# Kernel tuning notes

Hardware: AMD Instinct MI355X
Metric: run time of the kernel (lower is better)

Reference implementation:

```python
import jax, jax.numpy as jnp
import numpy as np

SLOPE = 25.0   # surrogate.fast_sigmoid(slope=25)
THRESH = 1.0   # snntorch default threshold
BN_EPS = 1e-5
LN_EPS = 1e-5

@jax.custom_vjp
def spike(x):
    return (x > 0).astype(x.dtype)

def _spike_fwd(x):
    return (x > 0).astype(x.dtype), x

def _spike_bwd(x, g):
    # fast_sigmoid surrogate gradient: 1 / (slope*|x| + 1)^2
    return (g / (SLOPE * jnp.abs(x) + 1.0) ** 2,)

spike.defvjp(_spike_fwd, _spike_bwd)

def lif(inp, mem, beta):
    # snntorch Leaky (reset_mechanism='subtract'):
    # reset from previous mem, then integrate, then fire
    reset = spike(mem - THRESH)
    mem = beta * mem + inp - reset * THRESH
    spk = spike(mem - THRESH)
    return spk, mem

def _forward(L_norm, X_seq, conv_w, conv_b, bn_gamma, bn_beta, bn_mean, bn_var,
             gcn1_w, gcn1_b, mask1, gcn2_w, gcn2_b, mask2, beta2,
             attn_w1, attn_b1, attn_w2, attn_b2,
             cls_w1, cls_b1, ln_gamma, ln_beta, cls_w2, cls_b2):
    B = X_seq.shape[0]
    N = L_norm.shape[1]            # 64 nodes
    # [B,T,N,1] -> [B,N,T]
    x = jnp.squeeze(X_seq, -1).transpose(0, 2, 1)
    # causal conv1d (pad left k-1=2) + inference BatchNorm1d
    y = jax.lax.conv_general_dilated(x, conv_w, (1,), [(2, 0)],
                                     dimension_numbers=('NCH', 'OIH', 'NCH'))
    y = y + conv_b[None, :, None]
    y = (y - bn_mean[None, :, None]) * (bn_gamma[None, :, None]
        * jax.lax.rsqrt(bn_var[None, :, None] + BN_EPS)) + bn_beta[None, :, None]
    # dynamic Laplacian masks (constant across steps -> hoisted out of scan)
    m1 = jax.nn.sigmoid(mask1 + mask1.T) * 0.5
    m2 = jax.nn.sigmoid(mask2 + mask2.T) * 0.5
    L1 = L_norm * m1[None]         # [B,N,N]
    L2 = L_norm * m2[None]
    xs = y.transpose(2, 0, 1)[..., None]   # [T,B,N,1]

    def step(carry, xt):
        mem_t, mem_g1, mem_g2 = carry
        spk_t, mem_t = lif(xt, mem_t, 0.9)
        cur1 = jnp.einsum('bij,bjf->bif', L1, spk_t @ gcn1_w) + gcn1_b
        spk1, mem_g1 = lif(cur1, mem_g1, 0.85)
        cur2 = jnp.einsum('bij,bjf->bif', L2, spk1 @ gcn2_w) + gcn2_b
        spk2, mem_g2 = lif(cur2, mem_g2, beta2)
        return (mem_t, mem_g1, mem_g2), mem_g2.reshape(B, -1)

    init = (jnp.zeros((B, N, 1), x.dtype),
            jnp.zeros((B, N, 16), x.dtype),
            jnp.zeros((B, N, 32), x.dtype))
    _, pots = jax.lax.scan(step, init, xs)       # [T,B,N*32]
    pots = pots.transpose(1, 0, 2)               # [B,T,2048]
    # temporal attention decoder
    scores = jnp.tanh(pots @ attn_w1 + attn_b1) @ attn_w2 + attn_b2  # [B,T,1]
    w = jax.nn.softmax(scores, axis=1)
    ctx = jnp.sum(pots * w, axis=1)              # [B,2048]
    h = ctx @ cls_w1 + cls_b1                    # [B,128]
    mu = jnp.mean(h, axis=-1, keepdims=True)
    var = jnp.var(h, axis=-1, keepdims=True)
    h = (h - mu) * jax.lax.rsqrt(var + LN_EPS) * ln_gamma + ln_beta
    h = jax.nn.gelu(h, approximate=False)        # dropout is identity at eval
    return h @ cls_w2 + cls_b2                   # [B,4]

def setup_inputs() -> dict:
    key = jax.random.key(0)
    ks = jax.random.split(key, 16)
    B, T, N = 4096, 15, 64
    f32 = jnp.float32
    def xavier(k, shape):
        lim = float(np.sqrt(6.0 / (shape[0] + shape[1])))
        return jax.random.uniform(k, shape, f32, -lim, lim)
    return {
        'L_norm': jax.random.normal(ks[0], (B, N, N), f32),
        'X_seq': jax.random.normal(ks[1], (B, T, N, 1), f32),
        'conv_w': jax.random.normal(ks[2], (64, 64, 3), f32) / np.sqrt(64 * 3),
        'conv_b': jnp.zeros((64,), f32),
        'bn_gamma': jnp.ones((64,), f32),
        'bn_beta': jnp.zeros((64,), f32),
        'bn_mean': jnp.zeros((64,), f32),
        'bn_var': jnp.ones((64,), f32),
        'gcn1_w': xavier(ks[3], (1, 16)),
        'gcn1_b': jnp.zeros((16,), f32),
        'mask1': jnp.ones((N, N), f32),
        'gcn2_w': xavier(ks[4], (16, 32)),
        'gcn2_b': jnp.zeros((32,), f32),
        'mask2': jnp.ones((N, N), f32),
        'beta2': jnp.asarray(0.9, f32),
        'attn_w1': xavier(ks[5], (2048, 32)),
        'attn_b1': jnp.zeros((32,), f32),
        'attn_w2': xavier(ks[6], (32, 1)),
        'attn_b2': jnp.zeros((1,), f32),
        'cls_w1': xavier(ks[7], (2048, 128)),
        'cls_b1': jnp.zeros((128,), f32),
        'ln_gamma': jnp.ones((128,), f32),
        'ln_beta': jnp.zeros((128,), f32),
        'cls_w2': xavier(ks[8], (128, 4)),
        'cls_b2': jnp.zeros((4,), f32),
    }

def reference(L_norm, X_seq, conv_w, conv_b, bn_gamma, bn_beta, bn_mean, bn_var,
              gcn1_w, gcn1_b, mask1, gcn2_w, gcn2_b, mask2, beta2,
              attn_w1, attn_b1, attn_w2, attn_b2,
              cls_w1, cls_b1, ln_gamma, ln_beta, cls_w2, cls_b2):
    return _forward(L_norm, X_seq, conv_w, conv_b, bn_gamma, bn_beta, bn_mean, bn_var,
                    gcn1_w, gcn1_b, mask1, gcn2_w, gcn2_b, mask2, beta2,
                    attn_w1, attn_b1, attn_w2, attn_b2,
                    cls_w1, cls_b1, ln_gamma, ln_beta, cls_w2, cls_b2)
```

## Files before the change

### kernel.cpp

```cpp
#include <hip/hip_runtime.h>
#include <math.h>

#define WS_M1_F    0
#define WS_M2_F    4096
#define WS_BNSC_F  8192
#define WS_BNSH_F  8256
#define WS_WT_F    8448
#define OFF_W1T    83968
#define OFF_CW1H   215040
#define OFF_CW1L   739328
#define OFF_CTX    1263616

typedef _Float16 v8h __attribute__((ext_vector_type(8)));
typedef short v8s __attribute__((ext_vector_type(8)));
typedef float v4f __attribute__((ext_vector_type(4)));
typedef float v16f __attribute__((ext_vector_type(16)));

__device__ __forceinline__ unsigned short f2h_u(float x) {
  _Float16 h = (_Float16)x;
  union { _Float16 h; unsigned short u; } v; v.h = h; return v.u;
}
__device__ __forceinline__ unsigned short bf16t(float x) {
  union { float f; unsigned int u; } v; v.f = x; return (unsigned short)(v.u >> 16);
}
__device__ __forceinline__ float bf16tof(unsigned short s) {
  union { unsigned int u; float f; } v; v.u = ((unsigned int)s) << 16; return v.f;
}

__global__ __launch_bounds__(256) void k_prep(
    const float* __restrict__ mask1, const float* __restrict__ mask2,
    const float* __restrict__ conv_w, const float* __restrict__ conv_b,
    const float* __restrict__ bn_gamma, const float* __restrict__ bn_beta,
    const float* __restrict__ bn_mean, const float* __restrict__ bn_var,
    const float* __restrict__ attn_w1, const float* __restrict__ cls_w1,
    float* __restrict__ wsf, unsigned short* __restrict__ w1t,
    unsigned short* __restrict__ cw1h, unsigned short* __restrict__ cw1l)
{
  const int gid = blockIdx.x * 256 + threadIdx.x;
  const int gsz = gridDim.x * 256;
  float* m1 = wsf + WS_M1_F;
  float* m2 = wsf + WS_M2_F;
  float* bnsc = wsf + WS_BNSC_F;
  float* bnsh = wsf + WS_BNSH_F;
  float* wT = wsf + WS_WT_F;
  for (int e = gid; e < 4096; e += gsz) {
    int i = e >> 6, j = e & 63;
    float s1 = mask1[e] + mask1[j * 64 + i];
    float s2 = mask2[e] + mask2[j * 64 + i];
    m1[e] = 0.5f / (1.f + expf(-s1));
    m2[e] = 0.5f / (1.f + expf(-s2));
  }
  for (int e = gid; e < 64; e += gsz) {
    float sc = bn_gamma[e] * rsqrtf(bn_var[e] + 1e-5f);
    bnsc[e] = sc;
    bnsh[e] = (conv_b[e] - bn_mean[e]) * sc + bn_beta[e];
  }
  for (int e = gid; e < 12288; e += gsz) {
    int o = e / 192, ik = e % 192;
    wT[ik * 64 + o] = conv_w[e];
  }
  for (int e = gid; e < 65536; e += gsz) {
    int n = e >> 11, i = e & 2047;
    w1t[e] = f2h_u(attn_w1[i * 32 + n]);
  }
  for (int e = gid; e < 262144; e += gsz) {
    int n = e >> 11, k = e & 2047;
    float x = cls_w1[k * 128 + n];
    unsigned short h = bf16t(x);
    cw1h[e] = h;
    cw1l[e] = bf16t(x - bf16tof(h));
  }
}

__global__ __launch_bounds__(256) void k_fused(
    const float* __restrict__ L_norm, const float* __restrict__ X_seq,
    const float* __restrict__ gcn1_w, const float* __restrict__ gcn1_b,
    const float* __restrict__ gcn2_w, const float* __restrict__ gcn2_b,
    const float* __restrict__ beta2p, const float* __restrict__ wsf,
    const unsigned short* __restrict__ w1t,
    const float* __restrict__ attn_b1, const float* __restrict__ attn_w2,
    const float* __restrict__ attn_b2,
    unsigned short* __restrict__ ctxh, unsigned short* __restrict__ ctxl,
    int b0)
{
  __shared__ __align__(16) unsigned short pots_s[16 * 2048];
  __shared__ __align__(16) char smR[11776];
  float* xcur = (float*)smR;
  float* zp = (float*)(smR + 3840);
  unsigned short* spk1T = (unsigned short*)(smR + 4352);
  float* Z2f = (float*)(smR + 6656);

  const int tid = threadIdx.x;
  const int lane = tid & 63;
  const int wv = tid >> 6;
  const int b = b0 + blockIdx.x;

  const float* m1 = wsf + WS_M1_F;
  const float* m2 = wsf + WS_M2_F;

  {
    float* xraw = (float*)pots_s;
    for (int e = tid; e < 960; e += 256) xraw[e] = X_seq[(size_t)b * 960 + e];
    *(uint4*)&pots_s[15 * 2048 + tid * 8] = make_uint4(0u, 0u, 0u, 0u);
    __syncthreads();
    const float* bnsc = wsf + WS_BNSC_F;
    const float* bnsh = wsf + WS_BNSH_F;
    const float* wT = wsf + WS_WT_F;
    const int o = lane;
    const int t0 = wv, t1 = wv + 4, t2 = wv + 8, t3 = wv + 12;
    float a0 = 0.f, a1 = 0.f, a2 = 0.f, a3 = 0.f;
    for (int i = 0; i < 64; ++i) {
      const float w0 = wT[(3 * i + 0) * 64 + o];
      const float w1 = wT[(3 * i + 1) * 64 + o];
      const float w2 = wT[(3 * i + 2) * 64 + o];
      float xa = (t0 >= 2) ? xraw[(t0 - 2) * 64 + i] : 0.f;
      float xb = (t0 >= 1) ? xraw[(t0 - 1) * 64 + i] : 0.f;
      a0 += w0 * xa + w1 * xb + w2 * xraw[t0 * 64 + i];
      a1 += w0 * xraw[(t1 - 2) * 64 + i] + w1 * xraw[(t1 - 1) * 64 + i] + w2 * xraw[t1 * 64 + i];
      a2 += w0 * xraw[(t2 - 2) * 64 + i] + w1 * xraw[(t2 - 1) * 64 + i] + w2 * xraw[t2 * 64 + i];
      if (t3 < 15)
        a3 += w0 * xraw[(t3 - 2) * 64 + i] + w1 * xraw[(t3 - 1) * 64 + i] + w2 * xraw[t3 * 64 + i];
    }
    const float sc = bnsc[o], sh = bnsh[o];
    xcur[t0 * 64 + o] = a0 * sc + sh;
    xcur[t1 * 64 + o] = a1 * sc + sh;
    xcur[t2 * 64 + o] = a2 * sc + sh;
    if (t3 < 15) xcur[t3 * 64 + o] = a3 * sc + sh;
    __syncthreads();
  }

  float L1h[32];
  const int kb1 = (wv & 1) * 32;
  if (wv >= 2) {
    const float* Lb = L_norm + (size_t)b * 4096 + lane * 64 + kb1;
    const float* mr = m1 + lane * 64 + kb1;
#pragma unroll
    for (int q4 = 0; q4 < 8; ++q4) {
      float4 lv = *(const float4*)(Lb + 4 * q4);
      float4 mv = *(const float4*)(mr + 4 * q4);
      L1h[4 * q4 + 0] = lv.x * mv.x;
      L1h[4 * q4 + 1] = lv.y * mv.y;
      L1h[4 * q4 + 2] = lv.z * mv.z;
      L1h[4 * q4 + 3] = lv.w * mv.w;
    }
  }

  v8s A_hi[2], A_lo[2];
  {
    const int irow = wv * 16 + (lane & 15);
    const int quad = (lane >> 4) & 3;
#pragma unroll
    for (int kb = 0; kb < 2; ++kb) {
      const float* Lb = L_norm + (size_t)b * 4096 + irow * 64 + kb * 32 + quad * 8;
      const float* mr = m2 + irow * 64 + kb * 32 + quad * 8;
      float4 la = *(const float4*)Lb, lb2 = *(const float4*)(Lb + 4);
      float4 ma = *(const float4*)mr, mb = *(const float4*)(mr + 4);
      float v[8] = { la.x * ma.x, la.y * ma.y, la.z * ma.z, la.w * ma.w,
                     lb2.x * mb.x, lb2.y * mb.y, lb2.z * mb.z, lb2.w * mb.w };
#pragma unroll
      for (int e = 0; e < 8; ++e) {
        unsigned short h = bf16t(v[e]);
        unsigned short l = bf16t(v[e] - bf16tof(h));
        A_hi[kb][e] = (short)h;
        A_lo[kb][e] = (short)l;
      }
    }
  }

  v8s W_hi, W_lo;
  {
    const int n = lane & 31;
    const int kh = (lane >> 5) & 1;
#pragma unroll
    for (int e = 0; e < 8; ++e) {
      float x = gcn2_w[(kh * 8 + e) * 32 + n];
      unsigned short h = bf16t(x);
      unsigned short l = bf16t(x - bf16tof(h));
      W_hi[e] = (short)h;
      W_lo[e] = (short)l;
    }
  }

  const float b2h = gcn2_b[lane & 31];
  const int np = tid >> 3;
  const int cp = tid & 7;
  float w1c[2], b1c[2];
#pragma unroll
  for (int d = 0; d < 2; ++d) { w1c[d] = gcn1_w[2 * cp + d]; b1c[d] = gcn1_b[2 * cp + d]; }
  const float beta2 = beta2p[0];

  float mem_t = 0.f;
  float mg1[4] = {0.f, 0.f, 0.f, 0.f};
  v16f mg2;
#pragma unroll
  for (int r = 0; r < 16; ++r) mg2[r] = 0.f;

  auto stage_b = [&](int tm1) {
    const int m = lane & 31;
    const int half = lane >> 5;
    const float* zr = Z2f + (wv * 32 + m) * 20 + half * 8;
    float4 za = *(const float4*)zr;
    float4 zb = *(const float4*)(zr + 4);
    float vv[8] = {za.x, za.y, za.z, za.w, zb.x, zb.y, zb.z, zb.w};
    v8s Ah, Al;
#pragma unroll
    for (int e = 0; e < 8; ++e) {
      unsigned short h = bf16t(vv[e]);
      unsigned short l = bf16t(vv[e] - bf16tof(h));
      Ah[e] = (short)h;
      Al[e] = (short)l;
    }
    v16f acc;
#pragma unroll
    for (int r = 0; r < 16; ++r) {
      float rs = (mg2[r] > 1.f) ? 1.f : 0.f;
      acc[r] = fmaf(beta2, mg2[r], b2h - rs);
    }
    acc = __builtin_amdgcn_mfma_f32_32x32x16_bf16(Ah, W_hi, acc, 0, 0, 0);
    acc = __builtin_amdgcn_mfma_f32_32x32x16_bf16(Al, W_hi, acc, 0, 0, 0);
    acc = __builtin_amdgcn_mfma_f32_32x32x16_bf16(Ah, W_lo, acc, 0, 0, 0);
    mg2 = acc;
    const int xorv = (tm1 & 7) << 3;
    const int base = tm1 * 2048 + m;
#pragma unroll
    for (int r = 0; r < 16; ++r) {
      int i = wv * 32 + (r & 3) + 8 * (r >> 2) + 4 * half;
      pots_s[(base + i * 32) ^ xorv] = f2h_u(acc[r]);
    }
  };

  for (int t = 0; t < 15; ++t) {
    if (wv >= 2) {
      float xc = xcur[t * 64 + lane];
      float rs = (mem_t > 1.f) ? 1.f : 0.f;
      mem_t = 0.9f * mem_t + xc - rs;
      float sp = (mem_t > 1.f) ? 1.f : 0.f;
      int spi = __float_as_int(sp);
      float zh = 0.f;
#pragma unroll
      for (int k = 0; k < 32; ++k) {
        float s = __int_as_float(__builtin_amdgcn_readlane(spi, kb1 + k));
        zh = fmaf(s, L1h[k], zh);
      }
      zp[(wv & 1) * 64 + lane] = zh;
    } else if (t > 0) {
      stage_b(t - 1);
    }
    __syncthreads();
    {
      float2 q0 = *(const float2*)&zp[2 * np];
      float2 q1 = *(const float2*)&zp[64 + 2 * np];
      float z0 = q0.x + q1.x;
      float z1v = q0.y + q1.y;
#pragma unroll
      for (int d = 0; d < 2; ++d) {
        float cur0 = fmaf(z0, w1c[d], b1c[d]);
        float rs0 = (mg1[d * 2 + 0] > 1.f) ? 1.f : 0.f;
        mg1[d * 2 + 0] = 0.85f * mg1[d * 2 + 0] + cur0 - rs0;
        unsigned int bits0 = (mg1[d * 2 + 0] > 1.f) ? 0x3F80u : 0u;
        float cur1 = fmaf(z1v, w1c[d], b1c[d]);
        float rs1 = (mg1[d * 2 + 1] > 1.f) ? 1.f : 0.f;
        mg1[d * 2 + 1] = 0.85f * mg1[d * 2 + 1] + cur1 - rs1;
        unsigned int bits1 = (mg1[d * 2 + 1] > 1.f) ? 0x3F80u : 0u;
        *(unsigned int*)&spk1T[(2 * cp + d) * 72 + 2 * np] = bits0 | (bits1 << 16);
      }
    }
    __syncthreads();
    {
      const int c = lane & 15;
      const int quad = (lane >> 4) & 3;
      const unsigned short* bp = spk1T + c * 72 + quad * 8;
      v8s B0 = *(const v8s*)(bp);
      v8s B1 = *(const v8s*)(bp + 32);
      v4f acc = {0.f, 0.f, 0.f, 0.f};
      acc = __builtin_amdgcn_mfma_f32_16x16x32_bf16(A_hi[0], B0, acc, 0, 0, 0);
      acc = __builtin_amdgcn_mfma_f32_16x16x32_bf16(A_lo[0], B0, acc, 0, 0, 0);
      acc = __builtin_amdgcn_mfma_f32_16x16x32_bf16(A_hi[1], B1, acc, 0, 0, 0);
      acc = __builtin_amdgcn_mfma_f32_16x16x32_bf16(A_lo[1], B1, acc, 0, 0, 0);
      const int r0 = wv * 16 + quad * 4;
#pragma unroll
      for (int r = 0; r < 4; ++r) Z2f[(r0 + r) * 20 + c] = acc[r];
    }
    __syncthreads();
  }
  if (wv < 2) stage_b(14);
  __syncthreads();

  float* sred = (float*)smR;
  float* wbuf = (float*)(smR + 8192);
  const int m = lane & 15;
  const int quad = lane >> 4;
  const int koff = quad * 8;

  v4f a0 = {0.f, 0.f, 0.f, 0.f}, a1 = {0.f, 0.f, 0.f, 0.f};
  {
    const int axor = (m & 7) << 3;
    const int abase = m * 2048 + koff;
    const unsigned short* B0p = w1t + (size_t)m * 2048 + koff;
    const unsigned short* B1p = w1t + (size_t)(m + 16) * 2048 + koff;
#pragma unroll 4
    for (int c = wv * 16; c < wv * 16 + 16; ++c) {
      v8h A = *(const v8h*)(pots_s + ((abase + c * 32) ^ axor));
      v8h B0 = *(const v8h*)(B0p + c * 32);
      v8h B1 = *(const v8h*)(B1p + c * 32);
      a0 = __builtin_amdgcn_mfma_f32_16x16x32_f16(A, B0, a0, 0, 0, 0);
      a1 = __builtin_amdgcn_mfma_f32_16x16x32_f16(A, B1, a1, 0, 0, 0);
    }
  }
#pragma unroll
  for (int j = 0; j < 4; ++j) {
    sred[j * 256 + tid] = a0[j];
    sred[(j + 4) * 256 + tid] = a1[j];
  }
  __syncthreads();
  float s0[4], s1[4];
#pragma unroll
  for (int j = 0; j < 4; ++j) {
    s0[j] = sred[j * 256 + 0 * 64 + lane] + sred[j * 256 + 1 * 64 + lane]
          + sred[j * 256 + 2 * 64 + lane] + sred[j * 256 + 3 * 64 + lane];
    s1[j] = sred[(j + 4) * 256 + 0 * 64 + lane] + sred[(j + 4) * 256 + 1 * 64 + lane]
          + sred[(j + 4) * 256 + 2 * 64 + lane] + sred[(j + 4) * 256 + 3 * 64 + lane];
  }
  float wlar[16];
  {
    const int n = m;
    const float b1a = attn_b1[n], b1b = attn_b1[n + 16];
    const float w2a = attn_w2[n], w2b = attn_w2[n + 16];
    const float b2 = attn_b2[0];
    float sc[4];
#pragma unroll
    for (int r = 0; r < 4; ++r) {
      float v = tanhf(s0[r] + b1a) * w2a + tanhf(s1[r] + b1b) * w2b;
      v += __shfl_xor(v, 1, 64);
      v += __shfl_xor(v, 2, 64);
      v += __shfl_xor(v, 4, 64);
      v += __shfl_xor(v, 8, 64);
      sc[r] = v + b2;
    }
    float mx = -1e30f;
#pragma unroll
    for (int r = 0; r < 4; ++r) if (quad * 4 + r < 15) mx = fmaxf(mx, sc[r]);
    mx = fmaxf(mx, __shfl_xor(mx, 16, 64));
    mx = fmaxf(mx, __shfl_xor(mx, 32, 64));
    float e[4], den = 0.f;
#pragma unroll
    for (int r = 0; r < 4; ++r) {
      e[r] = (quad * 4 + r < 15) ? expf(sc[r] - mx) : 0.f;
      den += e[r];
    }
    den += __shfl_xor(den, 16, 64);
    den += __shfl_xor(den, 32, 64);
    const float inv = 1.f / den;
    if ((lane & 15) == 0) {
      v4f wq = {e[0] * inv, e[1] * inv, e[2] * inv, e[3] * inv};
      *(v4f*)&wbuf[wv * 16 + quad * 4] = wq;
    }
#pragma unroll
    for (int q4 = 0; q4 < 4; ++q4) {
      float4 v = *(const float4*)&wbuf[wv * 16 + q4 * 4];
      wlar[q4 * 4 + 0] = v.x; wlar[q4 * 4 + 1] = v.y;
      wlar[q4 * 4 + 2] = v.z; wlar[q4 * 4 + 3] = v.w;
    }
  }
  float cv[8] = {0.f, 0.f, 0.f, 0.f, 0.f, 0.f, 0.f, 0.f};
#pragma unroll
  for (int t = 0; t < 15; ++t) {
    const int idx = (t * 2048 + tid * 8) ^ ((t & 7) << 3);
    v8h pv = *(const v8h*)(pots_s + idx);
    const float w = wlar[t];
#pragma unroll
    for (int j = 0; j < 8; ++j) cv[j] = fmaf(w, (float)pv[j], cv[j]);
  }
  unsigned short hv[8], lv[8];
#pragma unroll
  for (int j = 0; j < 8; ++j) {
    unsigned short h = bf16t(cv[j]);
    hv[j] = h;
    lv[j] = bf16t(cv[j] - bf16tof(h));
  }
  *(uint4*)(ctxh + (size_t)blockIdx.x * 2048 + tid * 8) = *(const uint4*)hv;
  *(uint4*)(ctxl + (size_t)blockIdx.x * 2048 + tid * 8) = *(const uint4*)lv;
}

__global__ __launch_bounds__(256) void k_cls(
    const unsigned short* __restrict__ ctxh, const unsigned short* __restrict__ ctxl,
    const unsigned short* __restrict__ cw1h, const unsigned short* __restrict__ cw1l,
    const float* __restrict__ cls_b1,
    const float* __restrict__ ln_g, const float* __restrict__ ln_b,
    const float* __restrict__ cls_w2, const float* __restrict__ cls_b2,
    float* __restrict__ out, int b0)
{
  __shared__ float hbuf[16 * 132];
  const int tid = threadIdx.x;
  const int lane = tid & 63;
  const int wv = tid >> 6;
  const int m = lane & 15;
  const int quad = lane >> 4;
  const int koff = quad * 8;
  const int r0l = blockIdx.x * 16;

  v4f a0 = {0.f, 0.f, 0.f, 0.f}, a1 = {0.f, 0.f, 0.f, 0.f};
  {
    const unsigned short* Ah = ctxh + (size_t)(r0l + m) * 2048;
    const unsigned short* Al = ctxl + (size_t)(r0l + m) * 2048;
    const int n0 = wv * 32 + m;
    const unsigned short* B0h = cw1h + (size_t)n0 * 2048;
    const unsigned short* B0l = cw1l + (size_t)n0 * 2048;
    const unsigned short* B1h = cw1h + (size_t)(n0 + 16) * 2048;
    const unsigned short* B1l = cw1l + (size_t)(n0 + 16) * 2048;
#pragma unroll 4
    for (int kc = 0; kc < 64; ++kc) {
      const int kb = kc * 32 + koff;
      v8s vAh = *(const v8s*)(Ah + kb);
      v8s vAl = *(const v8s*)(Al + kb);
      v8s vB0h = *(const v8s*)(B0h + kb);
      v8s vB0l = *(const v8s*)(B0l + kb);
      v8s vB1h = *(const v8s*)(B1h + kb);
      v8s vB1l = *(const v8s*)(B1l + kb);
      a0 = __builtin_amdgcn_mfma_f32_16x16x32_bf16(vAh, vB0h, a0, 0, 0, 0);
      a0 = __builtin_amdgcn_mfma_f32_16x16x32_bf16(vAl, vB0h, a0, 0, 0, 0);
      a0 = __builtin_amdgcn_mfma_f32_16x16x32_bf16(vAh, vB0l, a0, 0, 0, 0);
      a1 = __builtin_amdgcn_mfma_f32_16x16x32_bf16(vAh, vB1h, a1, 0, 0, 0);
      a1 = __builtin_amdgcn_mfma_f32_16x16x32_bf16(vAl, vB1h, a1, 0, 0, 0);
      a1 = __builtin_amdgcn_mfma_f32_16x16x32_bf16(vAh, vB1l, a1, 0, 0, 0);
    }
  }
  {
    const int n0 = wv * 32 + m;
    const float bb0 = cls_b1[n0], bb1 = cls_b1[n0 + 16];
#pragma unroll
    for (int r = 0; r < 4; ++r) {
      const int row = quad * 4 + r;
      hbuf[row * 132 + n0] = a0[r] + bb0;
      hbuf[row * 132 + n0 + 16] = a1[r] + bb1;
    }
  }
  __syncthreads();
  const float g0c = ln_g[lane], g1c = ln_g[lane + 64];
  const float b0c = ln_b[lane], b1c = ln_b[lane + 64];
  const float4 w2a = *(const float4*)(cls_w2 + lane * 4);
  const float4 w2b = *(const float4*)(cls_w2 + (lane + 64) * 4);
#pragma unroll
  for (int rr = 0; rr < 4; ++rr) {
    const int r = wv * 4 + rr;
    const float x0 = hbuf[r * 132 + lane];
    const float x1 = hbuf[r * 132 + 64 + lane];
    float s = x0 + x1, sq = x0 * x0 + x1 * x1;
#pragma unroll
    for (int mm = 32; mm >= 1; mm >>= 1) {
      s += __shfl_xor(s, mm, 64);
      sq += __shfl_xor(sq, mm, 64);
    }
    const float mu = s * (1.f / 128.f);
    const float var = sq * (1.f / 128.f) - mu * mu;
    const float rstd = rsqrtf(var + 1e-5f);
    float h0 = (x0 - mu) * rstd * g0c + b0c;
    float h1 = (x1 - mu) * rstd * g1c + b1c;
    h0 = 0.5f * h0 * (1.f + erff(h0 * 0.7071067811865475f));
    h1 = 0.5f * h1 * (1.f + erff(h1 * 0.7071067811865475f));
    float o0 = h0 * w2a.x + h1 * w2b.x;
    float o1 = h0 * w2a.y + h1 * w2b.y;
    float o2 = h0 * w2a.z + h1 * w2b.z;
    float o3 = h0 * w2a.w + h1 * w2b.w;
#pragma unroll
    for (int mm = 32; mm >= 1; mm >>= 1) {
      o0 += __shfl_xor(o0, mm, 64);
      o1 += __shfl_xor(o1, mm, 64);
      o2 += __shfl_xor(o2, mm, 64);
      o3 += __shfl_xor(o3, mm, 64);
    }
    if (lane == 0) {
      *(float4*)(out + (size_t)(b0 + r0l + r) * 4) =
          make_float4(o0 + cls_b2[0], o1 + cls_b2[1], o2 + cls_b2[2], o3 + cls_b2[3]);
    }
  }
}

extern "C" void kernel_launch(void* const* d_in, const int* in_sizes, int n_in,
                              void* d_out, int out_size, void* d_ws, size_t ws_size,
                              hipStream_t stream) {
  const float* L_norm   = (const float*)d_in[0];
  const float* X_seq    = (const float*)d_in[1];
  const float* conv_w   = (const float*)d_in[2];
  const float* conv_b   = (const float*)d_in[3];
  const float* bn_gamma = (const float*)d_in[4];
  const float* bn_beta  = (const float*)d_in[5];
  const float* bn_mean  = (const float*)d_in[6];
  const float* bn_var   = (const float*)d_in[7];
  const float* gcn1_w   = (const float*)d_in[8];
  const float* gcn1_b   = (const float*)d_in[9];
  const float* mask1    = (const float*)d_in[10];
  const float* gcn2_w   = (const float*)d_in[11];
  const float* gcn2_b   = (const float*)d_in[12];
  const float* mask2    = (const float*)d_in[13];
  const float* beta2    = (const float*)d_in[14];
  const float* attn_w1  = (const float*)d_in[15];
  const float* attn_b1  = (const float*)d_in[16];
  const float* attn_w2  = (const float*)d_in[17];
  const float* attn_b2  = (const float*)d_in[18];
  const float* cls_w1   = (const float*)d_in[19];
  const float* cls_b1   = (const float*)d_in[20];
  const float* ln_gamma = (const float*)d_in[21];
  const float* ln_beta  = (const float*)d_in[22];
  const float* cls_w2   = (const float*)d_in[23];
  const float* cls_b2   = (const float*)d_in[24];

  char* ws = (char*)d_ws;
  float* wsf = (float*)d_ws;
  unsigned short* w1t  = (unsigned short*)(ws + OFF_W1T);
  unsigned short* cw1h = (unsigned short*)(ws + OFF_CW1H);
  unsigned short* cw1l = (unsigned short*)(ws + OFF_CW1L);

  long long avail = (long long)ws_size - (long long)OFF_CTX;
  int chunk = 4096;
  if (avail < 8192LL * 4096LL) {
    long long c = (avail > 0) ? (avail / 8192) : 64;
    if (c > 4096) c = 4096;
    c &= ~63LL;
    if (c < 64) c = 64;
    chunk = (int)c;
  }
  unsigned short* ctxh = (unsigned short*)(ws + OFF_CTX);
  unsigned short* ctxl = ctxh + (size_t)chunk * 2048;

  hipLaunchKernelGGL(k_prep, dim3(64), dim3(256), 0, stream,
                     mask1, mask2, conv_w, conv_b, bn_gamma, bn_beta, bn_mean, bn_var,
                     attn_w1, cls_w1, wsf, w1t, cw1h, cw1l);

  for (int b0 = 0; b0 < 4096; b0 += chunk) {
    int cur = 4096 - b0;
    if (cur > chunk) cur = chunk;
    hipLaunchKernelGGL(k_fused, dim3(cur), dim3(256), 0, stream,
                       L_norm, X_seq, gcn1_w, gcn1_b, gcn2_w, gcn2_b, beta2,
                       wsf, w1t, attn_b1, attn_w2, attn_b2, ctxh, ctxl, b0);
    hipLaunchKernelGGL(k_cls, dim3(cur / 16), dim3(256), 0, stream,
                       ctxh, ctxl, cw1h, cw1l, cls_b1, ln_gamma, ln_beta, cls_w2, cls_b2,
                       (float*)d_out, b0);
  }
}
```

Before: 500.4 us.

## Double fused kernel block to 512 threads and split attention GEMM across eight waves

Raises the fused per-sample kernel from 256 to 512 threads. Waves 4-7 share the causal conv (one timestep per wave, weights staged in LDS) and take half of the attention-score MFMA K-loop, with a two-stage shared-memory reduction. The recurrent GCN stages stay on waves 0-3. The prep kernel now reads its inputs coalesced and scatters the transposed writes, runs on more blocks, and chunk sizes are balanced when workspace is limited. The larger block may reduce occupancy and adds a barrier, while most of the recurrent loop still runs on only half the waves.

```diff
diff --git a/kernel.cpp b/kernel.cpp
--- a/kernel.cpp
+++ b/kernel.cpp
@@ -59,20 +59,20 @@
     int o = e / 192, ik = e % 192;
     wT[ik * 64 + o] = conv_w[e];
   }
-  for (int e = gid; e < 65536; e += gsz) {
-    int n = e >> 11, i = e & 2047;
-    w1t[e] = f2h_u(attn_w1[i * 32 + n]);
-  }
-  for (int e = gid; e < 262144; e += gsz) {
-    int n = e >> 11, k = e & 2047;
-    float x = cls_w1[k * 128 + n];
+  for (int f = gid; f < 65536; f += gsz) {
+    int i = f >> 5, n = f & 31;
+    w1t[n * 2048 + i] = f2h_u(attn_w1[f]);
+  }
+  for (int f = gid; f < 262144; f += gsz) {
+    int k = f >> 7, n = f & 127;
+    float x = cls_w1[f];
     unsigned short h = bf16t(x);
-    cw1h[e] = h;
-    cw1l[e] = bf16t(x - bf16tof(h));
-  }
-}
-
-__global__ __launch_bounds__(256) void k_fused(
+    cw1h[n * 2048 + k] = h;
+    cw1l[n * 2048 + k] = bf16t(x - bf16tof(h));
+  }
+}
+
+__global__ __launch_bounds__(512) void k_fused(
     const float* __restrict__ L_norm, const float* __restrict__ X_seq,
     const float* __restrict__ gcn1_w, const float* __restrict__ gcn1_b,
     const float* __restrict__ gcn2_w, const float* __restrict__ gcn2_b,
@@ -100,38 +100,36 @@
 
   {
     float* xraw = (float*)pots_s;
-    for (int e = tid; e < 960; e += 256) xraw[e] = X_seq[(size_t)b * 960 + e];
-    *(uint4*)&pots_s[15 * 2048 + tid * 8] = make_uint4(0u, 0u, 0u, 0u);
+    float* wTl = (float*)(pots_s + 2048);
+    for (int e = tid; e < 960; e += 512) xraw[e] = X_seq[(size_t)b * 960 + e];
+    {
+      const float* wT = wsf + WS_WT_F;
+      for (int e = tid; e < 12288; e += 512) wTl[e] = wT[e];
+    }
+    if (tid < 256) *(uint4*)&pots_s[15 * 2048 + tid * 8] = make_uint4(0u, 0u, 0u, 0u);
     __syncthreads();
     const float* bnsc = wsf + WS_BNSC_F;
     const float* bnsh = wsf + WS_BNSH_F;
-    const float* wT = wsf + WS_WT_F;
     const int o = lane;
-    const int t0 = wv, t1 = wv + 4, t2 = wv + 8, t3 = wv + 12;
-    float a0 = 0.f, a1 = 0.f, a2 = 0.f, a3 = 0.f;
-    for (int i = 0; i < 64; ++i) {
-      const float w0 = wT[(3 * i + 0) * 64 + o];
-      const float w1 = wT[(3 * i + 1) * 64 + o];
-      const float w2 = wT[(3 * i + 2) * 64 + o];
-      float xa = (t0 >= 2) ? xraw[(t0 - 2) * 64 + i] : 0.f;
-      float xb = (t0 >= 1) ? xraw[(t0 - 1) * 64 + i] : 0.f;
-      a0 += w0 * xa + w1 * xb + w2 * xraw[t0 * 64 + i];
-      a1 += w0 * xraw[(t1 - 2) * 64 + i] + w1 * xraw[(t1 - 1) * 64 + i] + w2 * xraw[t1 * 64 + i];
-      a2 += w0 * xraw[(t2 - 2) * 64 + i] + w1 * xraw[(t2 - 1) * 64 + i] + w2 * xraw[t2 * 64 + i];
-      if (t3 < 15)
-        a3 += w0 * xraw[(t3 - 2) * 64 + i] + w1 * xraw[(t3 - 1) * 64 + i] + w2 * xraw[t3 * 64 + i];
-    }
     const float sc = bnsc[o], sh = bnsh[o];
-    xcur[t0 * 64 + o] = a0 * sc + sh;
-    xcur[t1 * 64 + o] = a1 * sc + sh;
-    xcur[t2 * 64 + o] = a2 * sc + sh;
-    if (t3 < 15) xcur[t3 * 64 + o] = a3 * sc + sh;
+    for (int tt = wv; tt < 15; tt += 8) {
+      float a = 0.f;
+      for (int i = 0; i < 64; ++i) {
+        const float w0 = wTl[(3 * i + 0) * 64 + o];
+        const float w1 = wTl[(3 * i + 1) * 64 + o];
+        const float w2 = wTl[(3 * i + 2) * 64 + o];
+        float xa = (tt >= 2) ? xraw[(tt - 2) * 64 + i] : 0.f;
+        float xb = (tt >= 1) ? xraw[(tt - 1) * 64 + i] : 0.f;
+        a += w0 * xa + w1 * xb + w2 * xraw[tt * 64 + i];
+      }
+      xcur[tt * 64 + o] = a * sc + sh;
+    }
     __syncthreads();
   }
 
   float L1h[32];
   const int kb1 = (wv & 1) * 32;
-  if (wv >= 2) {
+  if (wv == 2 || wv == 3) {
     const float* Lb = L_norm + (size_t)b * 4096 + lane * 64 + kb1;
     const float* mr = m1 + lane * 64 + kb1;
 #pragma unroll
@@ -146,7 +144,7 @@
   }
 
   v8s A_hi[2], A_lo[2];
-  {
+  if (wv < 4) {
     const int irow = wv * 16 + (lane & 15);
     const int quad = (lane >> 4) & 3;
 #pragma unroll
@@ -168,7 +166,7 @@
   }
 
   v8s W_hi, W_lo;
-  {
+  if (wv < 2) {
     const int n = lane & 31;
     const int kh = (lane >> 5) & 1;
 #pragma unroll
@@ -182,7 +180,7 @@
   }
 
   const float b2h = gcn2_b[lane & 31];
-  const int np = tid >> 3;
+  const int np = (tid & 255) >> 3;
   const int cp = tid & 7;
   float w1c[2], b1c[2];
 #pragma unroll
@@ -230,7 +228,7 @@
   };
 
   for (int t = 0; t < 15; ++t) {
-    if (wv >= 2) {
+    if (wv == 2 || wv == 3) {
       float xc = xcur[t * 64 + lane];
       float rs = (mem_t > 1.f) ? 1.f : 0.f;
       mem_t = 0.9f * mem_t + xc - rs;
@@ -243,11 +241,11 @@
         zh = fmaf(s, L1h[k], zh);
       }
       zp[(wv & 1) * 64 + lane] = zh;
-    } else if (t > 0) {
+    } else if (wv < 2 && t > 0) {
       stage_b(t - 1);
     }
     __syncthreads();
-    {
+    if (tid < 256) {
       float2 q0 = *(const float2*)&zp[2 * np];
       float2 q1 = *(const float2*)&zp[64 + 2 * np];
       float z0 = q0.x + q1.x;
@@ -266,7 +264,7 @@
       }
     }
     __syncthreads();
-    {
+    if (wv < 4) {
       const int c = lane & 15;
       const int quad = (lane >> 4) & 3;
       const unsigned short* bp = spk1T + c * 72 + quad * 8;
@@ -298,8 +296,8 @@
     const int abase = m * 2048 + koff;
     const unsigned short* B0p = w1t + (size_t)m * 2048 + koff;
     const unsigned short* B1p = w1t + (size_t)(m + 16) * 2048 + koff;
-#pragma unroll 4
-    for (int c = wv * 16; c < wv * 16 + 16; ++c) {
+#pragma unroll
+    for (int c = wv * 8; c < wv * 8 + 8; ++c) {
       v8h A = *(const v8h*)(pots_s + ((abase + c * 32) ^ axor));
       v8h B0 = *(const v8h*)(B0p + c * 32);
       v8h B1 = *(const v8h*)(B1p + c * 32);
@@ -307,79 +305,93 @@
       a1 = __builtin_amdgcn_mfma_f32_16x16x32_f16(A, B1, a1, 0, 0, 0);
     }
   }
-#pragma unroll
-  for (int j = 0; j < 4; ++j) {
-    sred[j * 256 + tid] = a0[j];
-    sred[(j + 4) * 256 + tid] = a1[j];
+  if (wv >= 4) {
+#pragma unroll
+    for (int j = 0; j < 4; ++j) {
+      sred[j * 256 + (wv - 4) * 64 + lane] = a0[j];
+      sred[(j + 4) * 256 + (wv - 4) * 64 + lane] = a1[j];
+    }
   }
   __syncthreads();
-  float s0[4], s1[4];
-#pragma unroll
-  for (int j = 0; j < 4; ++j) {
-    s0[j] = sred[j * 256 + 0 * 64 + lane] + sred[j * 256 + 1 * 64 + lane]
-          + sred[j * 256 + 2 * 64 + lane] + sred[j * 256 + 3 * 64 + lane];
-    s1[j] = sred[(j + 4) * 256 + 0 * 64 + lane] + sred[(j + 4) * 256 + 1 * 64 + lane]
-          + sred[(j + 4) * 256 + 2 * 64 + lane] + sred[(j + 4) * 256 + 3 * 64 + lane];
-  }
-  float wlar[16];
-  {
-    const int n = m;
-    const float b1a = attn_b1[n], b1b = attn_b1[n + 16];
-    const float w2a = attn_w2[n], w2b = attn_w2[n + 16];
-    const float b2 = attn_b2[0];
-    float sc[4];
-#pragma unroll
-    for (int r = 0; r < 4; ++r) {
-      float v = tanhf(s0[r] + b1a) * w2a + tanhf(s1[r] + b1b) * w2b;
-      v += __shfl_xor(v, 1, 64);
-      v += __shfl_xor(v, 2, 64);
-      v += __shfl_xor(v, 4, 64);
-      v += __shfl_xor(v, 8, 64);
-      sc[r] = v + b2;
-    }
-    float mx = -1e30f;
-#pragma unroll
-    for (int r = 0; r < 4; ++r) if (quad * 4 + r < 15) mx = fmaxf(mx, sc[r]);
-    mx = fmaxf(mx, __shfl_xor(mx, 16, 64));
-    mx = fmaxf(mx, __shfl_xor(mx, 32, 64));
-    float e[4], den = 0.f;
-#pragma unroll
-    for (int r = 0; r < 4; ++r) {
-      e[r] = (quad * 4 + r < 15) ? expf(sc[r] - mx) : 0.f;
-      den += e[r];
-    }
-    den += __shfl_xor(den, 16, 64);
-    den += __shfl_xor(den, 32, 64);
-    const float inv = 1.f / den;
-    if ((lane & 15) == 0) {
-      v4f wq = {e[0] * inv, e[1] * inv, e[2] * inv, e[3] * inv};
-      *(v4f*)&wbuf[wv * 16 + quad * 4] = wq;
-    }
-#pragma unroll
-    for (int q4 = 0; q4 < 4; ++q4) {
-      float4 v = *(const float4*)&wbuf[wv * 16 + q4 * 4];
-      wlar[q4 * 4 + 0] = v.x; wlar[q4 * 4 + 1] = v.y;
-      wlar[q4 * 4 + 2] = v.z; wlar[q4 * 4 + 3] = v.w;
-    }
-  }
-  float cv[8] = {0.f, 0.f, 0.f, 0.f, 0.f, 0.f, 0.f, 0.f};
-#pragma unroll
-  for (int t = 0; t < 15; ++t) {
-    const int idx = (t * 2048 + tid * 8) ^ ((t & 7) << 3);
-    v8h pv = *(const v8h*)(pots_s + idx);
-    const float w = wlar[t];
-#pragma unroll
-    for (int j = 0; j < 8; ++j) cv[j] = fmaf(w, (float)pv[j], cv[j]);
-  }
-  unsigned short hv[8], lv[8];
-#pragma unroll
-  for (int j = 0; j < 8; ++j) {
-    unsigned short h = bf16t(cv[j]);
-    hv[j] = h;
-    lv[j] = bf16t(cv[j] - bf16tof(h));
-  }
-  *(uint4*)(ctxh + (size_t)blockIdx.x * 2048 + tid * 8) = *(const uint4*)hv;
-  *(uint4*)(ctxl + (size_t)blockIdx.x * 2048 + tid * 8) = *(const uint4*)lv;
+  if (wv < 4) {
+#pragma unroll
+    for (int j = 0; j < 4; ++j) {
+      a0[j] += sred[j * 256 + wv * 64 + lane];
+      a1[j] += sred[(j + 4) * 256 + wv * 64 + lane];
+      sred[j * 256 + wv * 64 + lane] = a0[j];
+      sred[(j + 4) * 256 + wv * 64 + lane] = a1[j];
+    }
+  }
+  __syncthreads();
+  if (tid < 256) {
+    float s0[4], s1[4];
+#pragma unroll
+    for (int j = 0; j < 4; ++j) {
+      s0[j] = sred[j * 256 + 0 * 64 + lane] + sred[j * 256 + 1 * 64 + lane]
+            + sred[j * 256 + 2 * 64 + lane] + sred[j * 256 + 3 * 64 + lane];
+      s1[j] = sred[(j + 4) * 256 + 0 * 64 + lane] + sred[(j + 4) * 256 + 1 * 64 + lane]
+            + sred[(j + 4) * 256 + 2 * 64 + lane] + sred[(j + 4) * 256 + 3 * 64 + lane];
+    }
+    float wlar[16];
+    {
+      const int n = m;
+      const float b1a = attn_b1[n], b1b = attn_b1[n + 16];
+      const float w2a = attn_w2[n], w2b = attn_w2[n + 16];
+      const float b2 = attn_b2[0];
+      float sc[4];
+#pragma unroll
+      for (int r = 0; r < 4; ++r) {
+        float v = tanhf(s0[r] + b1a) * w2a + tanhf(s1[r] + b1b) * w2b;
+        v += __shfl_xor(v, 1, 64);
+        v += __shfl_xor(v, 2, 64);
+        v += __shfl_xor(v, 4, 64);
+        v += __shfl_xor(v, 8, 64);
+        sc[r] = v + b2;
+      }
+      float mx = -1e30f;
+#pragma unroll
+      for (int r = 0; r < 4; ++r) if (quad * 4 + r < 15) mx = fmaxf(mx, sc[r]);
+      mx = fmaxf(mx, __shfl_xor(mx, 16, 64));
+      mx = fmaxf(mx, __shfl_xor(mx, 32, 64));
+      float e[4], den = 0.f;
+#pragma unroll
+      for (int r = 0; r < 4; ++r) {
+        e[r] = (quad * 4 + r < 15) ? expf(sc[r] - mx) : 0.f;
+        den += e[r];
+      }
+      den += __shfl_xor(den, 16, 64);
+      den += __shfl_xor(den, 32, 64);
+      const float inv = 1.f / den;
+      if ((lane & 15) == 0) {
+        v4f wq = {e[0] * inv, e[1] * inv, e[2] * inv, e[3] * inv};
+        *(v4f*)&wbuf[wv * 16 + quad * 4] = wq;
+      }
+#pragma unroll
+      for (int q4 = 0; q4 < 4; ++q4) {
+        float4 v = *(const float4*)&wbuf[wv * 16 + q4 * 4];
+        wlar[q4 * 4 + 0] = v.x; wlar[q4 * 4 + 1] = v.y;
+        wlar[q4 * 4 + 2] = v.z; wlar[q4 * 4 + 3] = v.w;
+      }
+    }
+    float cv[8] = {0.f, 0.f, 0.f, 0.f, 0.f, 0.f, 0.f, 0.f};
+#pragma unroll
+    for (int t = 0; t < 15; ++t) {
+      const int idx = (t * 2048 + tid * 8) ^ ((t & 7) << 3);
+      v8h pv = *(const v8h*)(pots_s + idx);
+      const float w = wlar[t];
+#pragma unroll
+      for (int j = 0; j < 8; ++j) cv[j] = fmaf(w, (float)pv[j], cv[j]);
+    }
+    unsigned short hv[8], lv[8];
+#pragma unroll
+    for (int j = 0; j < 8; ++j) {
+      unsigned short h = bf16t(cv[j]);
+      hv[j] = h;
+      lv[j] = bf16t(cv[j] - bf16tof(h));
+    }
+    *(uint4*)(ctxh + (size_t)blockIdx.x * 2048 + tid * 8) = *(const uint4*)hv;
+    *(uint4*)(ctxl + (size_t)blockIdx.x * 2048 + tid * 8) = *(const uint4*)lv;
+  }
 }
 
 __global__ __launch_bounds__(256) void k_cls(
@@ -514,23 +526,27 @@
   long long avail = (long long)ws_size - (long long)OFF_CTX;
   int chunk = 4096;
   if (avail < 8192LL * 4096LL) {
-    long long c = (avail > 0) ? (avail / 8192) : 64;
-    if (c > 4096) c = 4096;
-    c &= ~63LL;
-    if (c < 64) c = 64;
-    chunk = (int)c;
+    long long cmax = (avail > 0) ? (avail / 8192) : 64;
+    if (cmax > 4096) cmax = 4096;
+    cmax &= ~63LL;
+    if (cmax < 64) cmax = 64;
+    int nch = (int)((4096 + cmax - 1) / cmax);
+    long long ceq = ((4096 / nch) + 63) & ~63LL;
+    while (ceq * nch < 4096) ceq += 64;
+    if (ceq > cmax) ceq = cmax;
+    chunk = (int)ceq;
   }
   unsigned short* ctxh = (unsigned short*)(ws + OFF_CTX);
   unsigned short* ctxl = ctxh + (size_t)chunk * 2048;
 
-  hipLaunchKernelGGL(k_prep, dim3(64), dim3(256), 0, stream,
+  hipLaunchKernelGGL(k_prep, dim3(256), dim3(256), 0, stream,
                      mask1, mask2, conv_w, conv_b, bn_gamma, bn_beta, bn_mean, bn_var,
                      attn_w1, cls_w1, wsf, w1t, cw1h, cw1l);
 
   for (int b0 = 0; b0 < 4096; b0 += chunk) {
     int cur = 4096 - b0;
     if (cur > chunk) cur = chunk;
-    hipLaunchKernelGGL(k_fused, dim3(cur), dim3(256), 0, stream,
+    hipLaunchKernelGGL(k_fused, dim3(cur), dim3(512), 0, stream,
                        L_norm, X_seq, gcn1_w, gcn1_b, gcn2_w, gcn2_b, beta2,
                        wsf, w1t, attn_b1, attn_w2, attn_b2, ctxh, ctxl, b0);
     hipLaunchKernelGGL(k_cls, dim3(cur / 16), dim3(256), 0, stream,
```

New measurement: 671.0 us. +34.1%, slower.

## Compute GCN1 spikes in MFMA B-fragment layout, drop smem transpose and barrier

Applied to the files above, without the earlier changes.

The GCN1 LIF update now runs directly in the lane layout that the MFMA B operand expects. Each lane keeps 16 membrane states and builds its bf16 spike fragments in registers, so the spk1T shared-memory transpose and one __syncthreads per timestep are gone. The trade is more redundant LIF work per lane and more registers. The prep kernel now reads its inputs coalesced and writes them scattered, and runs on 256 blocks instead of 64. Chunk sizing is also evened out when workspace is limited.

```diff
diff --git a/kernel.cpp b/kernel.cpp
--- a/kernel.cpp
+++ b/kernel.cpp
@@ -59,16 +59,16 @@
     int o = e / 192, ik = e % 192;
     wT[ik * 64 + o] = conv_w[e];
   }
-  for (int e = gid; e < 65536; e += gsz) {
-    int n = e >> 11, i = e & 2047;
-    w1t[e] = f2h_u(attn_w1[i * 32 + n]);
-  }
-  for (int e = gid; e < 262144; e += gsz) {
-    int n = e >> 11, k = e & 2047;
-    float x = cls_w1[k * 128 + n];
+  for (int f = gid; f < 65536; f += gsz) {
+    int i = f >> 5, n = f & 31;
+    w1t[n * 2048 + i] = f2h_u(attn_w1[f]);
+  }
+  for (int f = gid; f < 262144; f += gsz) {
+    int k = f >> 7, n = f & 127;
+    float x = cls_w1[f];
     unsigned short h = bf16t(x);
-    cw1h[e] = h;
-    cw1l[e] = bf16t(x - bf16tof(h));
+    cw1h[n * 2048 + k] = h;
+    cw1l[n * 2048 + k] = bf16t(x - bf16tof(h));
   }
 }
 
@@ -87,7 +87,6 @@
   __shared__ __align__(16) char smR[11776];
   float* xcur = (float*)smR;
   float* zp = (float*)(smR + 3840);
-  unsigned short* spk1T = (unsigned short*)(smR + 4352);
   float* Z2f = (float*)(smR + 6656);
 
   const int tid = threadIdx.x;
@@ -182,15 +181,18 @@
   }
 
   const float b2h = gcn2_b[lane & 31];
-  const int np = tid >> 3;
-  const int cp = tid & 7;
-  float w1c[2], b1c[2];
-#pragma unroll
-  for (int d = 0; d < 2; ++d) { w1c[d] = gcn1_w[2 * cp + d]; b1c[d] = gcn1_b[2 * cp + d]; }
   const float beta2 = beta2p[0];
 
+  const int c16 = lane & 15;
+  const int quad = (lane >> 4) & 3;
+  const int qa = quad * 8;
+  const float wcc = gcn1_w[c16];
+  const float bcc = gcn1_b[c16];
+  float mgA[8], mgB[8];
+#pragma unroll
+  for (int e = 0; e < 8; ++e) { mgA[e] = 0.f; mgB[e] = 0.f; }
+
   float mem_t = 0.f;
-  float mg1[4] = {0.f, 0.f, 0.f, 0.f};
   v16f mg2;
 #pragma unroll
   for (int r = 0; r < 16; ++r) mg2[r] = 0.f;
@@ -248,30 +250,30 @@
     }
     __syncthreads();
     {
-      float2 q0 = *(const float2*)&zp[2 * np];
-      float2 q1 = *(const float2*)&zp[64 + 2 * np];
-      float z0 = q0.x + q1.x;
-      float z1v = q0.y + q1.y;
-#pragma unroll
-      for (int d = 0; d < 2; ++d) {
-        float cur0 = fmaf(z0, w1c[d], b1c[d]);
-        float rs0 = (mg1[d * 2 + 0] > 1.f) ? 1.f : 0.f;
-        mg1[d * 2 + 0] = 0.85f * mg1[d * 2 + 0] + cur0 - rs0;
-        unsigned int bits0 = (mg1[d * 2 + 0] > 1.f) ? 0x3F80u : 0u;
-        float cur1 = fmaf(z1v, w1c[d], b1c[d]);
-        float rs1 = (mg1[d * 2 + 1] > 1.f) ? 1.f : 0.f;
-        mg1[d * 2 + 1] = 0.85f * mg1[d * 2 + 1] + cur1 - rs1;
-        unsigned int bits1 = (mg1[d * 2 + 1] > 1.f) ? 0x3F80u : 0u;
-        *(unsigned int*)&spk1T[(2 * cp + d) * 72 + 2 * np] = bits0 | (bits1 << 16);
+      float4 pa0 = *(const float4*)&zp[qa];
+      float4 pa1 = *(const float4*)&zp[qa + 4];
+      float4 pa2 = *(const float4*)&zp[64 + qa];
+      float4 pa3 = *(const float4*)&zp[68 + qa];
+      float4 pb0 = *(const float4*)&zp[32 + qa];
+      float4 pb1 = *(const float4*)&zp[36 + qa];
+      float4 pb2 = *(const float4*)&zp[96 + qa];
+      float4 pb3 = *(const float4*)&zp[100 + qa];
+      float zA[8] = {pa0.x + pa2.x, pa0.y + pa2.y, pa0.z + pa2.z, pa0.w + pa2.w,
+                     pa1.x + pa3.x, pa1.y + pa3.y, pa1.z + pa3.z, pa1.w + pa3.w};
+      float zB[8] = {pb0.x + pb2.x, pb0.y + pb2.y, pb0.z + pb2.z, pb0.w + pb2.w,
+                     pb1.x + pb3.x, pb1.y + pb3.y, pb1.z + pb3.z, pb1.w + pb3.w};
+      v8s B0, B1;
+#pragma unroll
+      for (int e = 0; e < 8; ++e) {
+        float curA = fmaf(zA[e], wcc, bcc);
+        float rsA = (mgA[e] > 1.f) ? 1.f : 0.f;
+        mgA[e] = 0.85f * mgA[e] + curA - rsA;
+        B0[e] = (mgA[e] > 1.f) ? (short)0x3F80 : (short)0;
+        float curB = fmaf(zB[e], wcc, bcc);
+        float rsB = (mgB[e] > 1.f) ? 1.f : 0.f;
+        mgB[e] = 0.85f * mgB[e] + curB - rsB;
+        B1[e] = (mgB[e] > 1.f) ? (short)0x3F80 : (short)0;
       }
-    }
-    __syncthreads();
-    {
-      const int c = lane & 15;
-      const int quad = (lane >> 4) & 3;
-      const unsigned short* bp = spk1T + c * 72 + quad * 8;
-      v8s B0 = *(const v8s*)(bp);
-      v8s B1 = *(const v8s*)(bp + 32);
       v4f acc = {0.f, 0.f, 0.f, 0.f};
       acc = __builtin_amdgcn_mfma_f32_16x16x32_bf16(A_hi[0], B0, acc, 0, 0, 0);
       acc = __builtin_amdgcn_mfma_f32_16x16x32_bf16(A_lo[0], B0, acc, 0, 0, 0);
@@ -279,7 +281,7 @@
       acc = __builtin_amdgcn_mfma_f32_16x16x32_bf16(A_lo[1], B1, acc, 0, 0, 0);
       const int r0 = wv * 16 + quad * 4;
 #pragma unroll
-      for (int r = 0; r < 4; ++r) Z2f[(r0 + r) * 20 + c] = acc[r];
+      for (int r = 0; r < 4; ++r) Z2f[(r0 + r) * 20 + c16] = acc[r];
     }
     __syncthreads();
   }
@@ -289,7 +291,6 @@
   float* sred = (float*)smR;
   float* wbuf = (float*)(smR + 8192);
   const int m = lane & 15;
-  const int quad = lane >> 4;
   const int koff = quad * 8;
 
   v4f a0 = {0.f, 0.f, 0.f, 0.f}, a1 = {0.f, 0.f, 0.f, 0.f};
@@ -514,16 +515,20 @@
   long long avail = (long long)ws_size - (long long)OFF_CTX;
   int chunk = 4096;
   if (avail < 8192LL * 4096LL) {
-    long long c = (avail > 0) ? (avail / 8192) : 64;
-    if (c > 4096) c = 4096;
-    c &= ~63LL;
-    if (c < 64) c = 64;
-    chunk = (int)c;
+    long long cmax = (avail > 0) ? (avail / 8192) : 64;
+    if (cmax > 4096) cmax = 4096;
+    cmax &= ~63LL;
+    if (cmax < 64) cmax = 64;
+    int nch = (int)((4096 + cmax - 1) / cmax);
+    long long ceq = ((4096 / nch) + 63) & ~63LL;
+    while (ceq * nch < 4096) ceq += 64;
+    if (ceq > cmax) ceq = cmax;
+    chunk = (int)ceq;
   }
   unsigned short* ctxh = (unsigned short*)(ws + OFF_CTX);
   unsigned short* ctxl = ctxh + (size_t)chunk * 2048;
 
-  hipLaunchKernelGGL(k_prep, dim3(64), dim3(256), 0, stream,
+  hipLaunchKernelGGL(k_prep, dim3(256), dim3(256), 0, stream,
                      mask1, mask2, conv_w, conv_b, bn_gamma, bn_beta, bn_mean, bn_var,
                      attn_w1, cls_w1, wsf, w1t, cw1h, cw1l);
 
```

Result: slower. 517.5 us (+3.4%).
